# Kernel optimization log

Measured on AMD Instinct MI355X. Metric: run time of the kernel, lower is better.

## Reference

```python
import jax, jax.numpy as jnp
import numpy as np
from jax import lax

DIST_THRESH = 180.0
ATT_THRESH = 0.05


def setup_inputs() -> dict:
    key = jax.random.key(0)
    ks = jax.random.split(key, 6)
    B, N, H, W = 16, 512, 25, 25
    F, Fh = H * W, int(H * W * 1.5)  # 625, 937
    x4 = jax.random.normal(ks[0], (B, N, H, W), dtype=jnp.float32) * 0.25
    attention = jax.random.uniform(ks[1], (B, N, 1, 1), dtype=jnp.float32)
    W1 = jax.random.normal(ks[2], (2, F, Fh), dtype=jnp.float32) * (1.0 / np.sqrt(F))
    b1 = jnp.zeros((Fh,), dtype=jnp.float32)
    W2 = jax.random.normal(ks[3], (2, Fh, F), dtype=jnp.float32) * (1.0 / np.sqrt(Fh))
    b2 = jnp.zeros((F,), dtype=jnp.float32)
    return {"x4": x4, "attention": attention, "W1": W1, "b1": b1, "W2": W2, "b2": b2}


def _build_adjacency(X, att):
    """X: [B,N,F] node features, att: [B,N]. Returns thresholded adjacency [B,N,N]."""
    B, N, F = X.shape
    # pairwise L1 distances, row-by-row scan to avoid materializing [B,N,N,F]
    Xs = jnp.swapaxes(X, 0, 1)  # [N,B,F]

    def row(_, xi):  # xi: [B,F]
        d = jnp.sum(jnp.abs(xi[:, None, :] - X), axis=-1)  # [B,N]
        return None, d

    _, D = lax.scan(row, None, Xs)          # [N,B,N]
    D = jnp.swapaxes(D, 0, 1)               # [B,N,N]
    att_d = jnp.abs(att[:, :, None] - att[:, None, :])  # [B,N,N]
    A = ((D <= DIST_THRESH) & (att_d <= ATT_THRESH)).astype(jnp.float32)
    # original only fills i<j and j<i, diagonal stays 0
    A = A * (1.0 - jnp.eye(N, dtype=jnp.float32))
    return A


def _process_graph(A):
    """A + I, then row-normalize by inverse degree (D^-1 (A+I))."""
    N = A.shape[1]
    A = A + jnp.eye(N, dtype=A.dtype)
    deg = jnp.sum(A, axis=-1)               # [B,N]
    dinv = jnp.where(deg > 0, 1.0 / deg, 0.0)
    return dinv[:, :, None] * A


def _cheb_conv(x, L, Wk, b):
    """ChebConv with K=2 over dense normalized graph L: T0=x, T1=Lx."""
    t1 = jnp.einsum('bij,bjf->bif', L, x)
    return jnp.einsum('bnf,fo->bno', x, Wk[0]) + jnp.einsum('bnf,fo->bno', t1, Wk[1]) + b


def reference(x4, attention, W1, b1, W2, b2):
    B, N, H, W = x4.shape
    X = x4.reshape(B, N, H * W)             # [B,N,625] flow_x
    att = attention[:, :, 0, 0]             # [B,N]
    A = _build_adjacency(X, att)
    L = _process_graph(A)
    h = jax.nn.relu(_cheb_conv(X, L, W1, b1))   # [B,N,937]
    out = jax.nn.relu(_cheb_conv(h, L, W2, b2))  # [B,N,625]
    return out
```

## Files before the change

kernel.cpp:

```cpp
#include <hip/hip_runtime.h>
#include <stdint.h>

typedef uint16_t u16;
typedef uint32_t u32;
typedef __attribute__((ext_vector_type(4))) float f32x4;
typedef __attribute__((ext_vector_type(4))) unsigned short us4;
typedef __attribute__((ext_vector_type(8))) unsigned short us8;

#define NB   16
#define NN   512
#define FF   625
#define FH   937
#define ROWS 8192
#define KS1  1280
#define KS2  1920
#define NPX  640
#define NPH  960
#define F4   160

using frag_ab = __attribute__((ext_vector_type(8))) short;
using frag_cd = __attribute__((ext_vector_type(4))) float;

__device__ __forceinline__ u16 f32_bf16(float f) {
  union { float f; uint32_t u; } x; x.f = f;
  uint32_t r = x.u + 0x7fffu + ((x.u >> 16) & 1u);
  return (u16)(r >> 16);
}
__device__ __forceinline__ void gload_lds16(const void* g, void* l) {
  __builtin_amdgcn_global_load_lds((__attribute__((address_space(1))) void*)g,
                                   (__attribute__((address_space(3))) void*)l,
                                   16, 0, 0);
}
__device__ __forceinline__ int swiz_row(int blk) {
  return ((blk & 7) << 10) | (blk >> 3);
}

__global__ __launch_bounds__(256) void prep(
    const float* __restrict__ x4, const float* __restrict__ W1,
    const float* __restrict__ W2, f32x4* __restrict__ Xpad,
    u16* __restrict__ Xcat, u16* __restrict__ Xt,
    u16* __restrict__ W1t, u16* __restrict__ W2t)
{
  const int blk = blockIdx.x;
  const int tid = threadIdx.x;
  if (blk < 4096) {
    const int xcd = blk & 7, loc = blk >> 3;
    const int row0 = xcd * 1024 + loc * 2;
    for (int s = tid; s < 320; s += 256) {
      const int row = row0 + (s >= 160);
      const int k4 = (s >= 160) ? s - 160 : s;
      f32x4 v; us4 o;
      #pragma unroll
      for (int t = 0; t < 4; ++t) {
        const int f = k4 * 4 + t;
        float x = (f < FF) ? x4[(size_t)row * FF + f] : 0.f;
        v[t] = x; o[t] = f32_bf16(x);
      }
      Xpad[(size_t)row * F4 + k4] = v;
      *(us4*)(Xcat + (size_t)row * KS1 + k4 * 4) = o;
    }
  } else if (blk < 9216) {
    __shared__ float tile[32][33];
    const int bb = blk - 4096;
    const int xcd = bb & 7, sub = bb >> 3;
    const int b = xcd * 2 + sub / 320;
    const int t = sub % 320;
    const int ft = t % 20, kt = t / 20;
    const int tx = tid & 31, ty = tid >> 5;
    #pragma unroll
    for (int r = 0; r < 4; ++r) {
      const int node = kt * 32 + ty + r * 8;
      const int f = ft * 32 + tx;
      tile[ty + r * 8][tx] = (f < FF) ? x4[((size_t)b * NN + node) * FF + f] : 0.f;
    }
    __syncthreads();
    #pragma unroll
    for (int r = 0; r < 4; ++r) {
      const int f = ft * 32 + ty + r * 8;
      const int node = kt * 32 + tx;
      Xt[((size_t)b * NPX + f) * 512 + node] = f32_bf16(tile[tx][ty + r * 8]);
    }
  } else if (blk < 10496) {
    __shared__ float tile[32][33];
    const int bb = blk - 9216;
    const int kt = bb % 40, nt = bb / 40;
    const int tx = tid & 31, ty = tid >> 5;
    #pragma unroll
    for (int r = 0; r < 4; ++r) {
      int k = kt * 32 + ty + r * 8;
      int n = nt * 32 + tx;
      float v = 0.f;
      int c = -1, kk = 0;
      if (k < 625) { c = 0; kk = k; }
      else if (k >= 640 && k < 1265) { c = 1; kk = k - 640; }
      if (c >= 0 && n < FH) v = W1[((size_t)c * 625 + kk) * FH + n];
      tile[ty + r * 8][tx] = v;
    }
    __syncthreads();
    #pragma unroll
    for (int r = 0; r < 4; ++r) {
      int n = nt * 32 + ty + r * 8;
      int k = kt * 32 + tx;
      W1t[(size_t)n * KS1 + k] = f32_bf16(tile[tx][ty + r * 8]);
    }
  } else {
    __shared__ float tile[32][33];
    const int bb = blk - 10496;
    const int kt = bb % 60, nt = bb / 60;
    const int tx = tid & 31, ty = tid >> 5;
    #pragma unroll
    for (int r = 0; r < 4; ++r) {
      int k = kt * 32 + ty + r * 8;
      int n = nt * 32 + tx;
      float v = 0.f;
      int c = -1, kk = 0;
      if (k < 937) { c = 0; kk = k; }
      else if (k >= 960 && k < 1897) { c = 1; kk = k - 960; }
      if (c >= 0 && n < FF) v = W2[((size_t)c * 937 + kk) * FF + n];
      tile[ty + r * 8][tx] = v;
    }
    __syncthreads();
    #pragma unroll
    for (int r = 0; r < 4; ++r) {
      int n = nt * 32 + ty + r * 8;
      int k = kt * 32 + tx;
      W2t[(size_t)n * KS2 + k] = f32_bf16(tile[tx][ty + r * 8]);
    }
  }
}

__global__ __launch_bounds__(256) void build_L(
    const f32x4* __restrict__ Xpad,
    const float* __restrict__ att,
    u16* __restrict__ L)
{
  __shared__ float att_sh[512];
  __shared__ f32x4 Xi4[F4];
  __shared__ u16 cand[512];
  __shared__ u16 flag[512];
  __shared__ int ncand, nacc;

  const int tid = threadIdx.x;
  const int row = swiz_row(blockIdx.x);
  const int b = row >> 9;
  const int i = row & 511;
  const f32x4* Xb4 = Xpad + (size_t)b * NN * F4;

  att_sh[tid]       = att[b * NN + tid];
  att_sh[tid + 256] = att[b * NN + tid + 256];
  if (tid < F4) Xi4[tid] = Xb4[(size_t)i * F4 + tid];
  flag[tid] = 0; flag[tid + 256] = 0;
  if (tid == 0) { ncand = 0; nacc = 0; }
  __syncthreads();

  const float ai = att_sh[i];
  for (int j = tid; j < NN; j += 256) {
    if (j != i && fabsf(ai - att_sh[j]) <= 0.05f) {
      int p = atomicAdd(&ncand, 1);
      cand[p] = (u16)j;
    }
  }
  __syncthreads();
  if (tid == 0) flag[i] = 1;

  const int hl = tid & 31;
  const int hw = tid >> 5;
  const int nc = ncand;

  const f32x4 a0 = Xi4[hl];
  const f32x4 a1 = Xi4[32 + hl];
  const f32x4 a2 = Xi4[64 + hl];
  const f32x4 a3 = Xi4[96 + hl];
  const f32x4 a4 = Xi4[128 + hl];

  for (int c = hw; c < nc; c += 8) {
    const int j = cand[c];
    const f32x4* Xj = Xb4 + (size_t)j * F4;
    const f32x4 d0 = a0 - Xj[hl];
    const f32x4 d1 = a1 - Xj[32 + hl];
    const f32x4 d2 = a2 - Xj[64 + hl];
    const f32x4 d3 = a3 - Xj[96 + hl];
    const f32x4 d4 = a4 - Xj[128 + hl];
    float p = 0.f;
    #pragma unroll
    for (int t = 0; t < 4; ++t)
      p += fabsf(d0[t]) + fabsf(d1[t]) + fabsf(d2[t]) + fabsf(d3[t]) + fabsf(d4[t]);
    #pragma unroll
    for (int off = 16; off; off >>= 1) p += __shfl_xor(p, off, 64);
    if (hl == 0 && p <= 180.0f) {
      atomicAdd(&nacc, 1);
      flag[j] = 1;
    }
  }
  __syncthreads();

  const u16 dv = f32_bf16(1.0f / (float)(nacc + 1));
  const u32 lo = flag[2 * tid]     ? (u32)dv : 0u;
  const u32 hi = flag[2 * tid + 1] ? (u32)dv : 0u;
  *(u32*)(L + (size_t)row * 512 + 2 * tid) = lo | (hi << 16);
}

template <int KS, int NTILE, int NREAL, int NSTORE, bool RELU, bool BIAS, bool OUT_BF16>
__device__ __forceinline__ void gemm_core(
    const u16* __restrict__ At,
    const u16* __restrict__ Btt,
    const float* __restrict__ bias, void* __restrict__ C,
    long crow0, int col0, int ldc)
{
  constexpr int NI = NTILE / 32;
  constexpr int BR = NTILE / 32;
  __shared__ __align__(16) u16 Ash[128 * 64];
  __shared__ __align__(16) u16 Bsh[NTILE * 64];

  const int tid  = threadIdx.x;
  const int lane = tid & 63;
  const int wave = tid >> 6;
  const int wm = wave & 1, wn = wave >> 1;
  const int q = lane >> 4, l16 = lane & 15;

  const u16* pa[4]; const u16* pb[BR];
  #pragma unroll
  for (int r = 0; r < 4; ++r) {
    const int ci = r * 256 + tid;
    const int row = ci >> 3, cpos = ci & 7;
    pa[r] = At + (size_t)row * KS + (cpos ^ (row & 7)) * 8;
  }
  #pragma unroll
  for (int r = 0; r < BR; ++r) {
    const int ci = r * 256 + tid;
    const int row = ci >> 3, cpos = ci & 7;
    pb[r] = Btt + (size_t)row * KS + (cpos ^ (row & 7)) * 8;
  }
  const int wbase = (tid & 192) * 8;

  const frag_ab* fA[4][2]; const frag_ab* fB[NI][2];
  #pragma unroll
  for (int mi = 0; mi < 4; ++mi) {
    const int row = wm * 64 + mi * 16 + l16;
    fA[mi][0] = (const frag_ab*)&Ash[row * 64 + ((q    ) ^ (l16 & 7)) * 8];
    fA[mi][1] = (const frag_ab*)&Ash[row * 64 + ((q + 4) ^ (l16 & 7)) * 8];
  }
  #pragma unroll
  for (int ni = 0; ni < NI; ++ni) {
    const int row = wn * (NTILE / 2) + ni * 16 + l16;
    fB[ni][0] = (const frag_ab*)&Bsh[row * 64 + ((q    ) ^ (l16 & 7)) * 8];
    fB[ni][1] = (const frag_ab*)&Bsh[row * 64 + ((q + 4) ^ (l16 & 7)) * 8];
  }

  frag_cd acc[4][NI] = {};

  constexpr int KT = KS / 64;
  for (int kt = 0; kt < KT; ++kt) {
    __syncthreads();
    #pragma unroll
    for (int r = 0; r < 4; ++r) { gload_lds16(pa[r], &Ash[r * 2048 + wbase]); pa[r] += 64; }
    #pragma unroll
    for (int r = 0; r < BR; ++r) { gload_lds16(pb[r], &Bsh[r * 2048 + wbase]); pb[r] += 64; }
    __syncthreads();

    #pragma unroll
    for (int kk = 0; kk < 2; ++kk) {
      frag_ab av[4], bv[NI];
      #pragma unroll
      for (int mi = 0; mi < 4; ++mi) av[mi] = *fA[mi][kk];
      #pragma unroll
      for (int ni = 0; ni < NI; ++ni) bv[ni] = *fB[ni][kk];
      #pragma unroll
      for (int mi = 0; mi < 4; ++mi)
        #pragma unroll
        for (int ni = 0; ni < NI; ++ni)
          acc[mi][ni] = __builtin_amdgcn_mfma_f32_16x16x32_bf16(
              av[mi], bv[ni], acc[mi][ni], 0, 0, 0);
    }
  }

  #pragma unroll
  for (int ni = 0; ni < NI; ++ni) {
    const int col = col0 + wn * (NTILE / 2) + ni * 16 + l16;
    if (col >= NSTORE) continue;
    const bool ok = (col < NREAL);
    float bvv = 0.f;
    if (BIAS) bvv = ok ? bias[col] : 0.f;
    #pragma unroll
    for (int mi = 0; mi < 4; ++mi) {
      #pragma unroll
      for (int r = 0; r < 4; ++r) {
        const long rowg = crow0 + wm * 64 + mi * 16 + q * 4 + r;
        float v = acc[mi][ni][r];
        if (BIAS) v += bvv;
        if (RELU) v = fmaxf(v, 0.f);
        if (!ok) v = 0.f;
        if (OUT_BF16) ((u16*)C)[rowg * (size_t)ldc + col] = f32_bf16(v);
        else          ((float*)C)[rowg * (size_t)ldc + col] = v;
      }
    }
  }
}

template <int KS, int NTILE, int NREAL, int NSTORE, bool RELU, bool BIAS, bool OUT_BF16>
__global__ __launch_bounds__(256) void gemm_dense(
    const u16* __restrict__ A, const u16* __restrict__ Bt,
    const float* __restrict__ bias, void* __restrict__ C, int ldc)
{
  const int x = blockIdx.x;
  const int mt = ((x & 7) << 3) | (x >> 3);
  gemm_core<KS, NTILE, NREAL, NSTORE, RELU, BIAS, OUT_BF16>(
      A + (size_t)mt * 128 * KS, Bt + (size_t)blockIdx.y * NTILE * KS,
      bias, C, (long)mt * 128, blockIdx.y * NTILE, ldc);
}

template <int NP>
__global__ __launch_bounds__(256) void spmm(
    const u16* __restrict__ L, const u16* __restrict__ Bt,
    u16* __restrict__ C, int ldc)
{
  constexpr int TPB = 4 * (NP / 64);
  const int blk = blockIdx.x;
  const int xcd = blk & 7, sub = blk >> 3;
  const int b = xcd * 2 + sub / TPB;
  const int t = sub % TPB;
  const int mt = t & 3, nt = t >> 2;
  gemm_core<512, 64, NP, NP, false, false, true>(
      L + ((size_t)b * 512 + mt * 128) * 512,
      Bt + ((size_t)b * NP + nt * 64) * 512,
      nullptr, C, (long)b * 512 + mt * 128, nt * 64, ldc);
}

__global__ __launch_bounds__(256) void transpose_h(
    const u16* __restrict__ hcat, u16* __restrict__ ht)
{
  __shared__ u16 tile[32][34];
  const int blk = blockIdx.x;
  const int xcd = blk & 7, sub = blk >> 3;
  const int b = xcd * 2 + sub / 480;
  const int t = sub % 480;
  const int kt = t % 16, nt = t / 16;
  const int tid = threadIdx.x;
  const int tx = tid & 31, ty = tid >> 5;
  #pragma unroll
  for (int r = 0; r < 4; ++r) {
    const int node = kt * 32 + ty + r * 8;
    const int n = nt * 32 + tx;
    tile[ty + r * 8][tx] = hcat[((size_t)b * NN + node) * KS2 + n];
  }
  __syncthreads();
  #pragma unroll
  for (int r = 0; r < 4; ++r) {
    const int n = nt * 32 + ty + r * 8;
    const int node = kt * 32 + tx;
    ht[((size_t)b * NPH + n) * 512 + node] = tile[tx][ty + r * 8];
  }
}

extern "C" void kernel_launch(void* const* d_in, const int* in_sizes, int n_in,
                              void* d_out, int out_size, void* d_ws, size_t ws_size,
                              hipStream_t stream) {
  const float* x4  = (const float*)d_in[0];
  const float* att = (const float*)d_in[1];
  const float* W1  = (const float*)d_in[2];
  const float* b1  = (const float*)d_in[3];
  const float* W2  = (const float*)d_in[4];
  const float* b2  = (const float*)d_in[5];
  float* out = (float*)d_out;

  char* ws = (char*)d_ws;
  f32x4* Xpad = (f32x4*)ws;
  u16* ht = (u16*)ws;       ws += (size_t)ROWS * F4 * 16;
  u16* Xcat = (u16*)ws;  ws += (size_t)ROWS * KS1 * 2;
  u16* hcat = (u16*)ws;  ws += (size_t)ROWS * KS2 * 2;
  u16* W1t  = (u16*)ws;  ws += (size_t)1024 * KS1 * 2;
  u16* W2t  = (u16*)ws;  ws += (size_t)640 * KS2 * 2;
  u16* Lm   = (u16*)ws;  ws += (size_t)NB * 512 * 512 * 2;
  u16* Xt   = (u16*)ws;  ws += (size_t)NB * NPX * 512 * 2;

  prep<<<dim3(11696), 256, 0, stream>>>(x4, W1, W2, Xpad, Xcat, Xt, W1t, W2t);
  build_L<<<dim3(ROWS), 256, 0, stream>>>(Xpad, att, Lm);
  spmm<NPX><<<dim3(640), 256, 0, stream>>>(Lm, Xt, Xcat + NPX, KS1);
  gemm_dense<KS1, 128, FH, NPH, true, true, true><<<dim3(64, 8), 256, 0, stream>>>(
      Xcat, W1t, b1, (void*)hcat, KS2);
  transpose_h<<<dim3(7680), 256, 0, stream>>>(hcat, ht);
  spmm<NPH><<<dim3(960), 256, 0, stream>>>(Lm, ht, hcat + NPH, KS2);
  gemm_dense<KS2, 64, FF, FF, true, true, false><<<dim3(64, 10), 256, 0, stream>>>(
      hcat, W2t, b2, (void*)out, FF);
}
```

Measured before the change: 222.3 us.

## Sort nodes by attention and build four adjacency rows per block

The prep kernel now ranks each batch's nodes by attention value and writes a sorted order plus sorted attention. build_L then assigns each block four nodes that are adjacent in that order. It gathers one shared candidate window with a ballot-based compaction and loads each candidate's features once to compare them against all four rows in registers. The aim is to cut redundant global reads of neighbour feature rows and reduce the block count by four. The cost is a larger, conservative candidate set for the group and more registers per thread, which may lower occupancy.

Result: slower. 238.1 us (+7.1%).

```diff
diff --git a/kernel.cpp b/kernel.cpp
--- a/kernel.cpp
+++ b/kernel.cpp
@@ -17,6 +17,7 @@
 #define NPX  640
 #define NPH  960
 #define F4   160
+#define GQ   4
 
 using frag_ab = __attribute__((ext_vector_type(8))) short;
 using frag_cd = __attribute__((ext_vector_type(4))) float;
@@ -31,15 +32,13 @@
                                    (__attribute__((address_space(3))) void*)l,
                                    16, 0, 0);
 }
-__device__ __forceinline__ int swiz_row(int blk) {
-  return ((blk & 7) << 10) | (blk >> 3);
-}
 
 __global__ __launch_bounds__(256) void prep(
-    const float* __restrict__ x4, const float* __restrict__ W1,
-    const float* __restrict__ W2, f32x4* __restrict__ Xpad,
-    u16* __restrict__ Xcat, u16* __restrict__ Xt,
-    u16* __restrict__ W1t, u16* __restrict__ W2t)
+    const float* __restrict__ x4, const float* __restrict__ att,
+    const float* __restrict__ W1, const float* __restrict__ W2,
+    f32x4* __restrict__ Xpad, u16* __restrict__ Xcat, u16* __restrict__ Xt,
+    u16* __restrict__ W1t, u16* __restrict__ W2t,
+    u16* __restrict__ order, float* __restrict__ att_s)
 {
   const int blk = blockIdx.x;
   const int tid = threadIdx.x;
@@ -103,7 +102,7 @@
       int k = kt * 32 + tx;
       W1t[(size_t)n * KS1 + k] = f32_bf16(tile[tx][ty + r * 8]);
     }
-  } else {
+  } else if (blk < 11696) {
     __shared__ float tile[32][33];
     const int bb = blk - 10496;
     const int kt = bb % 60, nt = bb / 60;
@@ -126,78 +125,140 @@
       int k = kt * 32 + tx;
       W2t[(size_t)n * KS2 + k] = f32_bf16(tile[tx][ty + r * 8]);
     }
+  } else {
+    __shared__ float a_sh[512];
+    const int b = blk - 11696;
+    a_sh[tid]       = att[b * NN + tid];
+    a_sh[tid + 256] = att[b * NN + tid + 256];
+    __syncthreads();
+    #pragma unroll
+    for (int h = 0; h < 2; ++h) {
+      const int i = tid + h * 256;
+      const float ai = a_sh[i];
+      int r = 0;
+      for (int j = 0; j < NN; ++j) {
+        const float aj = a_sh[j];
+        r += (aj < ai) || (aj == ai && j < i);
+      }
+      order[(size_t)b * NN + r] = (u16)i;
+      att_s[(size_t)b * NN + r] = ai;
+    }
   }
 }
 
 __global__ __launch_bounds__(256) void build_L(
     const f32x4* __restrict__ Xpad,
-    const float* __restrict__ att,
+    const u16* __restrict__ order,
+    const float* __restrict__ att_s,
     u16* __restrict__ L)
 {
-  __shared__ float att_sh[512];
-  __shared__ f32x4 Xi4[F4];
+  __shared__ float atts[512];
+  __shared__ u16 ords[512];
   __shared__ u16 cand[512];
-  __shared__ u16 flag[512];
-  __shared__ int ncand, nacc;
+  __shared__ u16 flag[GQ][512];
+  __shared__ int ncand, naccs[GQ];
 
   const int tid = threadIdx.x;
-  const int row = swiz_row(blockIdx.x);
-  const int b = row >> 9;
-  const int i = row & 511;
+  const int blk = blockIdx.x;
+  const int xcd = blk & 7, sub = blk >> 3;
+  const int b = xcd * 2 + (sub >> 7);
+  const int p0 = (sub & 127) * GQ;
   const f32x4* Xb4 = Xpad + (size_t)b * NN * F4;
 
-  att_sh[tid]       = att[b * NN + tid];
-  att_sh[tid + 256] = att[b * NN + tid + 256];
-  if (tid < F4) Xi4[tid] = Xb4[(size_t)i * F4 + tid];
-  flag[tid] = 0; flag[tid + 256] = 0;
-  if (tid == 0) { ncand = 0; nacc = 0; }
+  atts[tid]       = att_s[b * NN + tid];
+  atts[tid + 256] = att_s[b * NN + tid + 256];
+  ords[tid]       = order[b * NN + tid];
+  ords[tid + 256] = order[b * NN + tid + 256];
+  {
+    u32* fz = (u32*)&flag[0][0];
+    #pragma unroll
+    for (int s = 0; s < GQ; ++s) fz[tid + s * 256] = 0;
+  }
+  if (tid == 0) ncand = 0;
+  if (tid < GQ) naccs[tid] = 0;
   __syncthreads();
 
-  const float ai = att_sh[i];
-  for (int j = tid; j < NN; j += 256) {
-    if (j != i && fabsf(ai - att_sh[j]) <= 0.05f) {
-      int p = atomicAdd(&ncand, 1);
-      cand[p] = (u16)j;
-    }
+  float av[GQ]; int ig[GQ];
+  #pragma unroll
+  for (int g = 0; g < GQ; ++g) { av[g] = atts[p0 + g]; ig[g] = ords[p0 + g]; }
+  if (tid < GQ) flag[tid][ords[p0 + tid]] = 1;
+
+  {
+    const float lo = av[0] - 0.0501f, hi = av[GQ - 1] + 0.0501f;
+    const bool q0 = (atts[tid] >= lo) && (atts[tid] <= hi);
+    const bool q1 = (atts[tid + 256] >= lo) && (atts[tid + 256] <= hi);
+    const unsigned long long m0 = __ballot(q0);
+    const unsigned long long m1 = __ballot(q1);
+    const int c0 = __popcll(m0);
+    const int c1 = __popcll(m1);
+    const int lane = tid & 63;
+    int base = 0;
+    if (lane == 0 && (c0 + c1)) base = atomicAdd(&ncand, c0 + c1);
+    base = __shfl(base, 0, 64);
+    const unsigned long long below = (1ull << lane) - 1ull;
+    if (q0) cand[base + __popcll(m0 & below)] = (u16)tid;
+    if (q1) cand[base + c0 + __popcll(m1 & below)] = (u16)(tid + 256);
   }
   __syncthreads();
-  if (tid == 0) flag[i] = 1;
+  const int nc = ncand;
 
   const int hl = tid & 31;
   const int hw = tid >> 5;
-  const int nc = ncand;
-
-  const f32x4 a0 = Xi4[hl];
-  const f32x4 a1 = Xi4[32 + hl];
-  const f32x4 a2 = Xi4[64 + hl];
-  const f32x4 a3 = Xi4[96 + hl];
-  const f32x4 a4 = Xi4[128 + hl];
+
+  f32x4 xi[GQ][5];
+  #pragma unroll
+  for (int g = 0; g < GQ; ++g) {
+    const f32x4* Xi = Xb4 + (size_t)ig[g] * F4;
+    #pragma unroll
+    for (int s = 0; s < 5; ++s) xi[g][s] = Xi[s * 32 + hl];
+  }
 
   for (int c = hw; c < nc; c += 8) {
-    const int j = cand[c];
+    const int p = cand[c];
+    const int j = ords[p];
+    const float aj = atts[p];
     const f32x4* Xj = Xb4 + (size_t)j * F4;
-    const f32x4 d0 = a0 - Xj[hl];
-    const f32x4 d1 = a1 - Xj[32 + hl];
-    const f32x4 d2 = a2 - Xj[64 + hl];
-    const f32x4 d3 = a3 - Xj[96 + hl];
-    const f32x4 d4 = a4 - Xj[128 + hl];
-    float p = 0.f;
-    #pragma unroll
-    for (int t = 0; t < 4; ++t)
-      p += fabsf(d0[t]) + fabsf(d1[t]) + fabsf(d2[t]) + fabsf(d3[t]) + fabsf(d4[t]);
-    #pragma unroll
-    for (int off = 16; off; off >>= 1) p += __shfl_xor(p, off, 64);
-    if (hl == 0 && p <= 180.0f) {
-      atomicAdd(&nacc, 1);
-      flag[j] = 1;
+    f32x4 xj[5];
+    #pragma unroll
+    for (int s = 0; s < 5; ++s) xj[s] = Xj[s * 32 + hl];
+
+    float pd[GQ];
+    #pragma unroll
+    for (int g = 0; g < GQ; ++g) {
+      float p2 = 0.f;
+      #pragma unroll
+      for (int t = 0; t < 4; ++t) {
+        p2 += fabsf(xi[g][0][t] - xj[0][t]) + fabsf(xi[g][1][t] - xj[1][t])
+            + fabsf(xi[g][2][t] - xj[2][t]) + fabsf(xi[g][3][t] - xj[3][t])
+            + fabsf(xi[g][4][t] - xj[4][t]);
+      }
+      pd[g] = p2;
+    }
+    #pragma unroll
+    for (int off = 16; off; off >>= 1) {
+      #pragma unroll
+      for (int g = 0; g < GQ; ++g) pd[g] += __shfl_xor(pd[g], off, 64);
+    }
+    if (hl == 0) {
+      #pragma unroll
+      for (int g = 0; g < GQ; ++g) {
+        if (pd[g] <= 180.0f && fabsf(av[g] - aj) <= 0.05f && j != ig[g]) {
+          flag[g][j] = 1;
+          atomicAdd(&naccs[g], 1);
+        }
+      }
     }
   }
   __syncthreads();
 
-  const u16 dv = f32_bf16(1.0f / (float)(nacc + 1));
-  const u32 lo = flag[2 * tid]     ? (u32)dv : 0u;
-  const u32 hi = flag[2 * tid + 1] ? (u32)dv : 0u;
-  *(u32*)(L + (size_t)row * 512 + 2 * tid) = lo | (hi << 16);
+  #pragma unroll
+  for (int g = 0; g < GQ; ++g) {
+    const u16 dv = f32_bf16(1.0f / (float)(naccs[g] + 1));
+    const long row = (long)b * NN + ig[g];
+    const u32 lo2 = flag[g][2 * tid]     ? (u32)dv : 0u;
+    const u32 hi2 = flag[g][2 * tid + 1] ? (u32)dv : 0u;
+    *(u32*)(L + (size_t)row * 512 + 2 * tid) = lo2 | (hi2 << 16);
+  }
 }
 
 template <int KS, int NTILE, int NREAL, int NSTORE, bool RELU, bool BIAS, bool OUT_BF16>
@@ -372,9 +433,12 @@
   u16* W2t  = (u16*)ws;  ws += (size_t)640 * KS2 * 2;
   u16* Lm   = (u16*)ws;  ws += (size_t)NB * 512 * 512 * 2;
   u16* Xt   = (u16*)ws;  ws += (size_t)NB * NPX * 512 * 2;
-
-  prep<<<dim3(11696), 256, 0, stream>>>(x4, W1, W2, Xpad, Xcat, Xt, W1t, W2t);
-  build_L<<<dim3(ROWS), 256, 0, stream>>>(Xpad, att, Lm);
+  float* att_s = (float*)ws; ws += (size_t)NB * NN * 4;
+  u16* order_  = (u16*)ws;   ws += (size_t)NB * NN * 2;
+
+  prep<<<dim3(11712), 256, 0, stream>>>(x4, att, W1, W2, Xpad, Xcat, Xt,
+                                        W1t, W2t, order_, att_s);
+  build_L<<<dim3(2048), 256, 0, stream>>>(Xpad, order_, att_s, Lm);
   spmm<NPX><<<dim3(640), 256, 0, stream>>>(Lm, Xt, Xcat + NPX, KS1);
   gemm_dense<KS1, 128, FH, NPH, true, true, true><<<dim3(64, 8), 256, 0, stream>>>(
       Xcat, W1t, b1, (void*)hcat, KS2);
```
